# Optimization experiments

Hardware: AMD Instinct MI355X
Metric: run time of the kernel (lower is better)

Reference implementation:

```python
import jax, jax.numpy as jnp
import numpy as np

B, N, D = 512, 128, 128
VALID = 64                      # valid atoms per molecule (structured mask)
N_NODES = B * VALID             # 32768
DEG = 16
N_EDGES = N_NODES * DEG         # 524288
L = 3                           # predictor_layer_num
NUM_TASKS = 12
ATOM_VOCAB, EDGE_VOCAB = 119, 8


def _ln(x, g, b, eps=1e-5):
    mu = jnp.mean(x, -1, keepdims=True)
    v = jnp.mean((x - mu) ** 2, -1, keepdims=True)
    return (x - mu) * jax.lax.rsqrt(v + eps) * g + b


def _gelu(x):
    return jax.nn.gelu(x, approximate=False)  # torch F.gelu default (erf)


def setup_inputs():
    key = jax.random.key(0)
    ks = jax.random.split(key, 40)
    s = 0.02
    d = {}
    d['logits'] = jax.random.normal(ks[0], (B, N, D), jnp.float32)
    d['atom_mask'] = jnp.broadcast_to(jnp.arange(N) < VALID, (B, N))
    d['atom_feature'] = jax.random.randint(ks[1], (N_NODES,), 0, ATOM_VOCAB)
    d['edge_index'] = jax.random.randint(ks[2], (2, N_EDGES), 0, N_NODES)
    d['edge_attr'] = jax.random.randint(ks[3], (N_EDGES,), 0, EDGE_VOCAB)
    d['batch_idx'] = jnp.arange(N_NODES) // VALID
    # GNN encoder params
    d['atom_emb'] = s * jax.random.normal(ks[4], (ATOM_VOCAB, D))
    d['edge_emb'] = s * jax.random.normal(ks[5], (EDGE_VOCAB, D))
    d['gnn_W1'] = s * jax.random.normal(ks[6], (L, D, 2 * D))
    d['gnn_b1'] = jnp.zeros((L, 2 * D))
    d['gnn_W2'] = s * jax.random.normal(ks[7], (L, 2 * D, D))
    d['gnn_b2'] = jnp.zeros((L, D))
    d['gnn_ln_g'] = jnp.ones((L, D))
    d['gnn_ln_b'] = jnp.zeros((L, D))
    # attention pooling gate_nn: Linear(d,2d)->LN->ReLU->Linear(2d,1)
    d['gate_W1'] = s * jax.random.normal(ks[8], (D, 2 * D))
    d['gate_b1'] = jnp.zeros((2 * D,))
    d['gate_ln_g'] = jnp.ones((2 * D,))
    d['gate_ln_b'] = jnp.zeros((2 * D,))
    d['gate_W2'] = s * jax.random.normal(ks[9], (2 * D, 1))
    d['gate_b2'] = jnp.zeros((1,))
    # 2 residual blocks
    d['res_fc1_W'] = s * jax.random.normal(ks[10], (2, D, D))
    d['res_fc1_b'] = jnp.zeros((2, D))
    d['res_ln1_g'] = jnp.ones((2, D))
    d['res_ln1_b'] = jnp.zeros((2, D))
    d['res_fc2_W'] = s * jax.random.normal(ks[11], (2, D, D))
    d['res_fc2_b'] = jnp.zeros((2, D))
    d['res_ln2_g'] = jnp.ones((2, D))
    d['res_ln2_b'] = jnp.zeros((2, D))
    # prediction head
    d['pred_W1'] = s * jax.random.normal(ks[12], (D, D))
    d['pred_b1'] = jnp.zeros((D,))
    d['pred_W2'] = s * jax.random.normal(ks[13], (D, NUM_TASKS))
    d['pred_b2'] = jnp.zeros((NUM_TASKS,))
    return d


def reference(logits, atom_mask, atom_feature, edge_index, edge_attr, batch_idx,
              atom_emb, edge_emb, gnn_W1, gnn_b1, gnn_W2, gnn_b2, gnn_ln_g, gnn_ln_b,
              gate_W1, gate_b1, gate_ln_g, gate_ln_b, gate_W2, gate_b2,
              res_fc1_W, res_fc1_b, res_ln1_g, res_ln1_b,
              res_fc2_W, res_fc2_b, res_ln2_g, res_ln2_b,
              pred_W1, pred_b1, pred_W2, pred_b2):
    # boolean-mask gather: flat_atom_feat[flat_mask] with static masked count
    flat_mask = atom_mask.reshape(-1)
    idx = jnp.nonzero(flat_mask, size=N_NODES)[0]
    x = logits.reshape(-1, D)[idx]                       # [N_NODES, D]
    x = x + atom_emb[atom_feature]                       # incorporate atom features
    src, dst = edge_index[0], edge_index[1]
    e_emb = edge_emb[edge_attr]                          # [E, D]
    # residual GIN-style message passing, JK='last', eval (no dropout)
    for l in range(L):
        msg = jax.nn.relu(x[src] + e_emb)                # [E, D] irregular gather
        agg = jax.ops.segment_sum(msg, dst, num_segments=N_NODES)
        h = jax.nn.relu(agg @ gnn_W1[l] + gnn_b1[l]) @ gnn_W2[l] + gnn_b2[l]
        x = x + _ln(h, gnn_ln_g[l], gnn_ln_b[l])
    # attentional aggregation: segment softmax over nodes per graph
    gate = jax.nn.relu(_ln(x @ gate_W1 + gate_b1, gate_ln_g, gate_ln_b)) @ gate_W2 + gate_b2  # [n,1]
    gm = jax.ops.segment_max(gate, batch_idx, num_segments=B)
    e = jnp.exp(gate - gm[batch_idx])
    den = jax.ops.segment_sum(e, batch_idx, num_segments=B)
    w = e / den[batch_idx]
    g = jax.ops.segment_sum(w * x, batch_idx, num_segments=B)  # [B, D]
    # 2 residual MLP blocks (eval: dropout = identity)
    for r in range(2):
        h = _gelu(_ln(g @ res_fc1_W[r] + res_fc1_b[r], res_ln1_g[r], res_ln1_b[r]))
        h = _ln(h @ res_fc2_W[r] + res_fc2_b[r], res_ln2_g[r], res_ln2_b[r])
        g = g + h
    # prediction head
    return _gelu(g @ pred_W1 + pred_b1) @ pred_W2 + pred_b2  # [B, NUM_TASKS]
```

## Files before the change

### kernel.cpp

```cpp
#include <hip/hip_runtime.h>
#include <hip/hip_bf16.h>

#define N_NODES 32768
#define N_EDGES 524288
#define B_GRAPHS 512

typedef __attribute__((ext_vector_type(8))) short sh8;
typedef __attribute__((ext_vector_type(4))) float f32x4;

__device__ __forceinline__ unsigned short f2b(float f) {
    unsigned int u = __float_as_uint(f);
    return (unsigned short)((u + 0x7FFFu + ((u >> 16) & 1u)) >> 16);
}
__device__ __forceinline__ float blo(unsigned int u) { return __uint_as_float(u << 16); }
__device__ __forceinline__ float bhi(unsigned int u) { return __uint_as_float(u & 0xFFFF0000u); }
__device__ __forceinline__ float gelu_exact(float z) {
    return 0.5f * z * (1.0f + erff(z * 0.70710678118654752440f));
}

__global__ __launch_bounds__(256) void k_prep(const float* __restrict__ W1,
                                              const float* __restrict__ W2,
                                              const float* __restrict__ gW1,
                                              unsigned short* __restrict__ W1T,
                                              unsigned short* __restrict__ W2T,
                                              unsigned short* __restrict__ gW1T,
                                              int* __restrict__ deg) {
    int tid = blockIdx.x * 256 + threadIdx.x;
    if (tid < N_NODES) deg[tid] = 0;
    int m = tid >> 15, i = tid & 32767;
    if (m < 3) {
        int r = i >> 8, c = i & 255;
        W1T[m * 32768 + c * 128 + r] = f2b(W1[m * 32768 + i]);
    } else if (m < 6) {
        int mm = m - 3;
        int r = i >> 7, c = i & 127;
        W2T[mm * 32768 + c * 256 + r] = f2b(W2[mm * 32768 + i]);
    } else {
        int r = i >> 8, c = i & 255;
        gW1T[c * 128 + r] = f2b(gW1[i]);
    }
}

__global__ void k_deg(const int* __restrict__ dst, int* __restrict__ deg) {
    int e = blockIdx.x * blockDim.x + threadIdx.x;
    if (e < N_EDGES) atomicAdd(&deg[dst[e]], 1);
}

__global__ __launch_bounds__(1024) void k_scan(const int* __restrict__ deg,
                                               int* __restrict__ offs,
                                               int* __restrict__ cursor) {
    int tid = threadIdx.x;
    int lane = tid & 63, wid = tid >> 6;
    int base = tid * 32;
    int pref[32];
    int run = 0;
    #pragma unroll
    for (int i = 0; i < 32; i++) { pref[i] = run; run += deg[base + i]; }
    int s = run;
    for (int m = 1; m < 64; m <<= 1) { int t = __shfl_up(s, m); if (lane >= m) s += t; }
    __shared__ int wsum[16];
    if (lane == 63) wsum[wid] = s;
    __syncthreads();
    if (tid < 16) {
        int v = wsum[tid];
        for (int m = 1; m < 16; m <<= 1) { int t = __shfl_up(v, m, 16); if (tid >= m) v += t; }
        wsum[tid] = v;
    }
    __syncthreads();
    int wbase = wid ? wsum[wid - 1] : 0;
    int ebase = wbase + (s - run);
    #pragma unroll
    for (int i = 0; i < 32; i++) {
        int o = ebase + pref[i];
        offs[base + i] = o;
        cursor[base + i] = o;
    }
    if (tid == 1023) offs[N_NODES] = ebase + run;
}

__global__ void k_scatter(const int* __restrict__ src, const int* __restrict__ dst,
                          const int* __restrict__ attr, int* __restrict__ cursor,
                          int* __restrict__ csr) {
    int e = blockIdx.x * blockDim.x + threadIdx.x;
    if (e < N_EDGES) {
        int p = atomicAdd(&cursor[dst[e]], 1);
        csr[p] = src[e] | (attr[e] << 16);
    }
}

__global__ void k_build_x(const float* __restrict__ logits, const int* __restrict__ feat,
                          const float* __restrict__ aemb, float* __restrict__ x,
                          unsigned short* __restrict__ xb) {
    int idx = blockIdx.x * blockDim.x + threadIdx.x;
    int n = idx >> 5, c = idx & 31;
    int srow = ((n >> 6) << 7) + (n & 63);
    float4 lv = ((const float4*)logits)[srow * 32 + c];
    float4 av = ((const float4*)aemb)[feat[n] * 32 + c];
    float4 o;
    o.x = lv.x + av.x; o.y = lv.y + av.y; o.z = lv.z + av.z; o.w = lv.w + av.w;
    ((float4*)x)[idx] = o;
    ushort4 ob;
    ob.x = f2b(o.x); ob.y = f2b(o.y); ob.z = f2b(o.z); ob.w = f2b(o.w);
    ((ushort4*)xb)[idx] = ob;
}

__global__ __launch_bounds__(256) void k_agg(const unsigned short* __restrict__ xb,
                                             const int* __restrict__ offs,
                                             const int* __restrict__ csr,
                                             const float* __restrict__ eemb,
                                             unsigned short* __restrict__ aggb) {
    __shared__ float semb[8 * 128];
    int tid = threadIdx.x;
    for (int i = tid; i < 1024; i += 256) semb[i] = eemb[i];
    __syncthreads();
    int node = blockIdx.x * 4 + (tid >> 6);
    int lane = tid & 63;
    int li = lane & 31, h = lane >> 5;
    int o0 = offs[node], o1 = offs[node + 1];
    float a0 = 0.f, a1 = 0.f, a2 = 0.f, a3 = 0.f;
    int e = o0 + h;
    for (; e + 14 < o1; e += 16) {
        int p[8]; uint2 u[8]; float4 ev[8];
        #pragma unroll
        for (int j = 0; j < 8; j++) p[j] = csr[e + 2 * j];
        #pragma unroll
        for (int j = 0; j < 8; j++)
            u[j] = *(const uint2*)(xb + (size_t)(p[j] & 0xFFFF) * 128 + li * 4);
        #pragma unroll
        for (int j = 0; j < 8; j++)
            ev[j] = *(const float4*)&semb[(p[j] >> 16) * 128 + li * 4];
        #pragma unroll
        for (int j = 0; j < 8; j++) {
            a0 += fmaxf(blo(u[j].x) + ev[j].x, 0.f);
            a1 += fmaxf(bhi(u[j].x) + ev[j].y, 0.f);
            a2 += fmaxf(blo(u[j].y) + ev[j].z, 0.f);
            a3 += fmaxf(bhi(u[j].y) + ev[j].w, 0.f);
        }
    }
    for (; e + 6 < o1; e += 8) {
        int p[4]; uint2 u[4]; float4 ev[4];
        #pragma unroll
        for (int j = 0; j < 4; j++) p[j] = csr[e + 2 * j];
        #pragma unroll
        for (int j = 0; j < 4; j++)
            u[j] = *(const uint2*)(xb + (size_t)(p[j] & 0xFFFF) * 128 + li * 4);
        #pragma unroll
        for (int j = 0; j < 4; j++)
            ev[j] = *(const float4*)&semb[(p[j] >> 16) * 128 + li * 4];
        #pragma unroll
        for (int j = 0; j < 4; j++) {
            a0 += fmaxf(blo(u[j].x) + ev[j].x, 0.f);
            a1 += fmaxf(bhi(u[j].x) + ev[j].y, 0.f);
            a2 += fmaxf(blo(u[j].y) + ev[j].z, 0.f);
            a3 += fmaxf(bhi(u[j].y) + ev[j].w, 0.f);
        }
    }
    for (; e < o1; e += 2) {
        int pk = csr[e];
        uint2 u = *(const uint2*)(xb + (size_t)(pk & 0xFFFF) * 128 + li * 4);
        float4 ev = *(const float4*)&semb[(pk >> 16) * 128 + li * 4];
        a0 += fmaxf(blo(u.x) + ev.x, 0.f); a1 += fmaxf(bhi(u.x) + ev.y, 0.f);
        a2 += fmaxf(blo(u.y) + ev.z, 0.f); a3 += fmaxf(bhi(u.y) + ev.w, 0.f);
    }
    a0 += __shfl_xor(a0, 32); a1 += __shfl_xor(a1, 32);
    a2 += __shfl_xor(a2, 32); a3 += __shfl_xor(a3, 32);
    if (h == 0) {
        uint2 wv;
        wv.x = (unsigned int)f2b(a0) | ((unsigned int)f2b(a1) << 16);
        wv.y = (unsigned int)f2b(a2) | ((unsigned int)f2b(a3) << 16);
        *(uint2*)(aggb + (size_t)node * 128 + li * 4) = wv;
    }
}

__global__ __launch_bounds__(512) void k_layer(const unsigned short* __restrict__ A,
                                               const unsigned short* __restrict__ W1T,
                                               const float* __restrict__ b1,
                                               const unsigned short* __restrict__ W2T,
                                               const float* __restrict__ b2,
                                               const float* __restrict__ lng,
                                               const float* __restrict__ lnb,
                                               float* __restrict__ x,
                                               unsigned short* __restrict__ xb) {
    __shared__ __align__(16) unsigned short WS[33792];
    __shared__ __align__(16) unsigned short T[128][264];
    int tid = threadIdx.x;
    int row0 = blockIdx.x * 128;
    int l = tid & 63, w = tid >> 6;
    int fr = l & 15, hi = l >> 4, fk = hi * 8;
    sh8 afr[4];
    #pragma unroll
    for (int kc = 0; kc < 4; kc++)
        afr[kc] = *(const sh8*)(A + (size_t)(row0 + w * 16 + fr) * 128 + kc * 32 + fk);
    #pragma unroll
    for (int s = tid; s < 4096; s += 512) {
        int n = s >> 4, k8 = s & 15;
        *(uint4*)&WS[n * 132 + k8 * 8] = *(const uint4*)(W1T + (size_t)n * 128 + k8 * 8);
    }
    __syncthreads();
    #pragma unroll
    for (int ch = 0; ch < 2; ch++) {
        f32x4 acc[8];
        #pragma unroll
        for (int c = 0; c < 8; c++) acc[c] = (f32x4){0.f, 0.f, 0.f, 0.f};
        #pragma unroll
        for (int kc = 0; kc < 4; kc++) {
            #pragma unroll
            for (int c = 0; c < 8; c++) {
                sh8 b = *(const sh8*)&WS[(ch * 128 + c * 16 + fr) * 132 + kc * 32 + fk];
                acc[c] = __builtin_amdgcn_mfma_f32_16x16x32_bf16(afr[kc], b, acc[c], 0, 0, 0);
            }
        }
        int rb = w * 16 + hi * 4;
        #pragma unroll
        for (int c = 0; c < 8; c++) {
            int col = ch * 128 + c * 16 + fr;
            float bv = b1[col];
            #pragma unroll
            for (int q = 0; q < 4; q++)
                T[rb + q][col] = f2b(fmaxf(acc[c][q] + bv, 0.f));
        }
    }
    __syncthreads();
    #pragma unroll
    for (int s = tid; s < 4096; s += 512) {
        int n = s >> 5, k8 = s & 31;
        *(uint4*)&WS[n * 264 + k8 * 8] = *(const uint4*)(W2T + (size_t)n * 256 + k8 * 8);
    }
    __syncthreads();
    f32x4 acc[8];
    #pragma unroll
    for (int c = 0; c < 8; c++) acc[c] = (f32x4){0.f, 0.f, 0.f, 0.f};
    #pragma unroll 2
    for (int kc = 0; kc < 8; kc++) {
        sh8 a = *(const sh8*)&T[w * 16 + fr][kc * 32 + fk];
        #pragma unroll
        for (int c = 0; c < 8; c++) {
            sh8 b = *(const sh8*)&WS[(c * 16 + fr) * 264 + kc * 32 + fk];
            acc[c] = __builtin_amdgcn_mfma_f32_16x16x32_bf16(a, b, acc[c], 0, 0, 0);
        }
    }
    float s0 = 0.f, s1 = 0.f, s2 = 0.f, s3 = 0.f;
    float q0 = 0.f, q1 = 0.f, q2 = 0.f, q3 = 0.f;
    #pragma unroll
    for (int c = 0; c < 8; c++) {
        float bv = b2[c * 16 + fr];
        #pragma unroll
        for (int q = 0; q < 4; q++) acc[c][q] += bv;
        s0 += acc[c][0]; q0 += acc[c][0] * acc[c][0];
        s1 += acc[c][1]; q1 += acc[c][1] * acc[c][1];
        s2 += acc[c][2]; q2 += acc[c][2] * acc[c][2];
        s3 += acc[c][3]; q3 += acc[c][3] * acc[c][3];
    }
    #pragma unroll
    for (int m = 1; m < 16; m <<= 1) {
        s0 += __shfl_xor(s0, m); q0 += __shfl_xor(q0, m);
        s1 += __shfl_xor(s1, m); q1 += __shfl_xor(q1, m);
        s2 += __shfl_xor(s2, m); q2 += __shfl_xor(q2, m);
        s3 += __shfl_xor(s3, m); q3 += __shfl_xor(q3, m);
    }
    float mu[4], rs_[4];
    mu[0] = s0 * (1.f / 128.f); rs_[0] = rsqrtf(q0 * (1.f / 128.f) - mu[0] * mu[0] + 1e-5f);
    mu[1] = s1 * (1.f / 128.f); rs_[1] = rsqrtf(q1 * (1.f / 128.f) - mu[1] * mu[1] + 1e-5f);
    mu[2] = s2 * (1.f / 128.f); rs_[2] = rsqrtf(q2 * (1.f / 128.f) - mu[2] * mu[2] + 1e-5f);
    mu[3] = s3 * (1.f / 128.f); rs_[3] = rsqrtf(q3 * (1.f / 128.f) - mu[3] * mu[3] + 1e-5f);
    int rbase = row0 + w * 16 + hi * 4;
    #pragma unroll
    for (int c = 0; c < 8; c++) {
        int col = c * 16 + fr;
        float g = lng[col], bb = lnb[col];
        #pragma unroll
        for (int q = 0; q < 4; q++) {
            size_t idx = (size_t)(rbase + q) * 128 + col;
            float nx = x[idx] + (acc[c][q] - mu[q]) * rs_[q] * g + bb;
            x[idx] = nx;
            xb[idx] = f2b(nx);
        }
    }
}

__global__ __launch_bounds__(512) void k_gatef(const unsigned short* __restrict__ xbin,
                                               const unsigned short* __restrict__ gW1T,
                                               const float* __restrict__ b1,
                                               const float* __restrict__ lng,
                                               const float* __restrict__ lnb,
                                               const float* __restrict__ w2,
                                               const float* __restrict__ b2,
                                               float* __restrict__ gate) {
    __shared__ __align__(16) unsigned short WS[33792];
    __shared__ __align__(16) unsigned short T[128][264];
    int tid = threadIdx.x;
    int row0 = blockIdx.x * 128;
    int l = tid & 63, w = tid >> 6;
    int fr = l & 15, hi = l >> 4, fk = hi * 8;
    sh8 afr[4];
    #pragma unroll
    for (int kc = 0; kc < 4; kc++)
        afr[kc] = *(const sh8*)(xbin + (size_t)(row0 + w * 16 + fr) * 128 + kc * 32 + fk);
    #pragma unroll
    for (int s = tid; s < 4096; s += 512) {
        int n = s >> 4, k8 = s & 15;
        *(uint4*)&WS[n * 132 + k8 * 8] = *(const uint4*)(gW1T + (size_t)n * 128 + k8 * 8);
    }
    __syncthreads();
    #pragma unroll
    for (int ch = 0; ch < 2; ch++) {
        f32x4 acc[8];
        #pragma unroll
        for (int c = 0; c < 8; c++) acc[c] = (f32x4){0.f, 0.f, 0.f, 0.f};
        #pragma unroll
        for (int kc = 0; kc < 4; kc++) {
            #pragma unroll
            for (int c = 0; c < 8; c++) {
                sh8 b = *(const sh8*)&WS[(ch * 128 + c * 16 + fr) * 132 + kc * 32 + fk];
                acc[c] = __builtin_amdgcn_mfma_f32_16x16x32_bf16(afr[kc], b, acc[c], 0, 0, 0);
            }
        }
        int rb = w * 16 + hi * 4;
        #pragma unroll
        for (int c = 0; c < 8; c++) {
            int col = ch * 128 + c * 16 + fr;
            float bv = b1[col];
            #pragma unroll
            for (int q = 0; q < 4; q++)
                T[rb + q][col] = f2b(acc[c][q] + bv);
        }
    }
    __syncthreads();
    int row = tid >> 2, qd = tid & 3;
    float s = 0.f, sq = 0.f;
    #pragma unroll 4
    for (int j = 0; j < 16; j++) {
        uint2 u = *(const uint2*)&T[row][qd * 64 + j * 4];
        float v0 = blo(u.x), v1 = bhi(u.x), v2 = blo(u.y), v3 = bhi(u.y);
        s += v0 + v1 + v2 + v3;
        sq += v0 * v0 + v1 * v1 + v2 * v2 + v3 * v3;
    }
    s += __shfl_xor(s, 1); s += __shfl_xor(s, 2);
    sq += __shfl_xor(sq, 1); sq += __shfl_xor(sq, 2);
    float mu = s * (1.f / 256.f);
    float rcp = rsqrtf(sq * (1.f / 256.f) - mu * mu + 1e-5f);
    float acc = 0.f;
    #pragma unroll 4
    for (int j = 0; j < 16; j++) {
        int col = qd * 64 + j * 4;
        uint2 u = *(const uint2*)&T[row][col];
        float4 g4 = *(const float4*)&lng[col];
        float4 e4 = *(const float4*)&lnb[col];
        float4 w4 = *(const float4*)&w2[col];
        acc += fmaxf((blo(u.x) - mu) * rcp * g4.x + e4.x, 0.f) * w4.x;
        acc += fmaxf((bhi(u.x) - mu) * rcp * g4.y + e4.y, 0.f) * w4.y;
        acc += fmaxf((blo(u.y) - mu) * rcp * g4.z + e4.z, 0.f) * w4.z;
        acc += fmaxf((bhi(u.y) - mu) * rcp * g4.w + e4.w, 0.f) * w4.w;
    }
    acc += __shfl_xor(acc, 1); acc += __shfl_xor(acc, 2);
    if (qd == 0) gate[row0 + row] = acc + b2[0];
}

__global__ __launch_bounds__(256) void k_pool(const float* __restrict__ x,
                                              const float* __restrict__ gate,
                                              float* __restrict__ g) {
    __shared__ float sw[64];
    __shared__ float sacc[128];
    int b = blockIdx.x, tid = threadIdx.x;
    if (tid < 64) {
        float gv = gate[b * 64 + tid];
        float m = gv;
        #pragma unroll
        for (int mk = 1; mk < 64; mk <<= 1) m = fmaxf(m, __shfl_xor(m, mk));
        float e = expf(gv - m);
        float s = e;
        #pragma unroll
        for (int mk = 1; mk < 64; mk <<= 1) s += __shfl_xor(s, mk);
        sw[tid] = e / s;
    }
    __syncthreads();
    int d = tid & 127, h = tid >> 7;
    float acc = 0.f;
    for (int i = h * 32; i < h * 32 + 32; i++)
        acc += sw[i] * x[(size_t)(b * 64 + i) * 128 + d];
    if (h == 0) sacc[d] = acc;
    __syncthreads();
    if (h == 1) g[b * 128 + d] = sacc[d] + acc;
}

__global__ __launch_bounds__(128) void k_tail(const float* __restrict__ g_in,
        const float* __restrict__ fc1W, const float* __restrict__ fc1b,
        const float* __restrict__ ln1g, const float* __restrict__ ln1b,
        const float* __restrict__ fc2W, const float* __restrict__ fc2b,
        const float* __restrict__ ln2g, const float* __restrict__ ln2b,
        const float* __restrict__ pW1, const float* __restrict__ pb1,
        const float* __restrict__ pW2, const float* __restrict__ pb2,
        float* __restrict__ out) {
    __shared__ float sg[128], sh[128];
    __shared__ float ps[2], pq[2];
    int b = blockIdx.x, tid = threadIdx.x;
    int w = tid >> 6;
    sg[tid] = g_in[b * 128 + tid];
    __syncthreads();
    for (int r = 0; r < 2; r++) {
        const float* W1 = fc1W + r * 16384;
        float acc = fc1b[r * 128 + tid];
        for (int k = 0; k < 128; k++) acc += sg[k] * W1[k * 128 + tid];
        float s = acc, q = acc * acc;
        #pragma unroll
        for (int m = 1; m < 64; m <<= 1) { s += __shfl_xor(s, m); q += __shfl_xor(q, m); }
        __syncthreads();
        if ((tid & 63) == 0) { ps[w] = s; pq[w] = q; }
        __syncthreads();
        float S = ps[0] + ps[1], Q = pq[0] + pq[1];
        float mu = S * (1.f / 128.f);
        float var = Q * (1.f / 128.f) - mu * mu;
        float z = (acc - mu) * rsqrtf(var + 1e-5f) * ln1g[r * 128 + tid] + ln1b[r * 128 + tid];
        z = gelu_exact(z);
        __syncthreads();
        sh[tid] = z;
        __syncthreads();
        const float* W2 = fc2W + r * 16384;
        float acc2 = fc2b[r * 128 + tid];
        for (int k = 0; k < 128; k++) acc2 += sh[k] * W2[k * 128 + tid];
        s = acc2; q = acc2 * acc2;
        #pragma unroll
        for (int m = 1; m < 64; m <<= 1) { s += __shfl_xor(s, m); q += __shfl_xor(q, m); }
        __syncthreads();
        if ((tid & 63) == 0) { ps[w] = s; pq[w] = q; }
        __syncthreads();
        S = ps[0] + ps[1]; Q = pq[0] + pq[1];
        mu = S * (1.f / 128.f);
        var = Q * (1.f / 128.f) - mu * mu;
        float z2 = (acc2 - mu) * rsqrtf(var + 1e-5f) * ln2g[r * 128 + tid] + ln2b[r * 128 + tid];
        __syncthreads();
        sg[tid] = sg[tid] + z2;
        __syncthreads();
    }
    float acc = pb1[tid];
    for (int k = 0; k < 128; k++) acc += sg[k] * pW1[k * 128 + tid];
    __syncthreads();
    sh[tid] = gelu_exact(acc);
    __syncthreads();
    if (tid < 12) {
        float o = pb2[tid];
        for (int k = 0; k < 128; k++) o += sh[k] * pW2[k * 12 + tid];
        out[b * 12 + tid] = o;
    }
}

extern "C" void kernel_launch(void* const* d_in, const int* in_sizes, int n_in,
                              void* d_out, int out_size, void* d_ws, size_t ws_size,
                              hipStream_t stream) {
    const float* logits    = (const float*)d_in[0];
    const int*   atom_feat = (const int*)d_in[2];
    const int*   edge_src  = (const int*)d_in[3];
    const int*   edge_dst  = edge_src + N_EDGES;
    const int*   edge_attr = (const int*)d_in[4];
    const float* atom_emb  = (const float*)d_in[6];
    const float* edge_emb  = (const float*)d_in[7];
    const float* gnn_W1    = (const float*)d_in[8];
    const float* gnn_b1    = (const float*)d_in[9];
    const float* gnn_W2    = (const float*)d_in[10];
    const float* gnn_b2    = (const float*)d_in[11];
    const float* gnn_ln_g  = (const float*)d_in[12];
    const float* gnn_ln_b  = (const float*)d_in[13];
    const float* gate_W1   = (const float*)d_in[14];
    const float* gate_b1   = (const float*)d_in[15];
    const float* gate_ln_g = (const float*)d_in[16];
    const float* gate_ln_b = (const float*)d_in[17];
    const float* gate_W2   = (const float*)d_in[18];
    const float* gate_b2   = (const float*)d_in[19];
    const float* res_fc1_W = (const float*)d_in[20];
    const float* res_fc1_b = (const float*)d_in[21];
    const float* res_ln1_g = (const float*)d_in[22];
    const float* res_ln1_b = (const float*)d_in[23];
    const float* res_fc2_W = (const float*)d_in[24];
    const float* res_fc2_b = (const float*)d_in[25];
    const float* res_ln2_g = (const float*)d_in[26];
    const float* res_ln2_b = (const float*)d_in[27];
    const float* pred_W1   = (const float*)d_in[28];
    const float* pred_b1   = (const float*)d_in[29];
    const float* pred_W2   = (const float*)d_in[30];
    const float* pred_b2   = (const float*)d_in[31];
    float* out = (float*)d_out;

    char* w = (char*)d_ws;
    float*          x    = (float*)w;          w += (size_t)N_NODES * 128 * 4;
    unsigned short* xb   = (unsigned short*)w; w += (size_t)N_NODES * 128 * 2;
    unsigned short* aggb = (unsigned short*)w; w += (size_t)N_NODES * 128 * 2;
    unsigned short* W1T  = (unsigned short*)w; w += 3 * 32768 * 2;
    unsigned short* W2T  = (unsigned short*)w; w += 3 * 32768 * 2;
    unsigned short* gW1T = (unsigned short*)w; w += 32768 * 2;
    int*   deg    = (int*)w;   w += N_NODES * 4;
    int*   offs   = (int*)w;   w += (N_NODES + 64) * 4;
    int*   cursor = (int*)w;   w += N_NODES * 4;
    int*   csr    = (int*)w;   w += N_EDGES * 4;
    float* gate   = (float*)w; w += N_NODES * 4;
    float* gpool  = (float*)w; w += B_GRAPHS * 128 * 4;

    k_prep<<<7 * 32768 / 256, 256, 0, stream>>>(gnn_W1, gnn_W2, gate_W1, W1T, W2T, gW1T, deg);
    k_deg<<<N_EDGES / 256, 256, 0, stream>>>(edge_dst, deg);
    k_scan<<<1, 1024, 0, stream>>>(deg, offs, cursor);
    k_scatter<<<N_EDGES / 256, 256, 0, stream>>>(edge_src, edge_dst, edge_attr, cursor, csr);

    k_build_x<<<N_NODES * 32 / 256, 256, 0, stream>>>(logits, atom_feat, atom_emb, x, xb);

    for (int l = 0; l < 3; l++) {
        k_agg<<<N_NODES / 4, 256, 0, stream>>>(xb, offs, csr, edge_emb, aggb);
        k_layer<<<N_NODES / 128, 512, 0, stream>>>(
            aggb, W1T + l * 32768, gnn_b1 + l * 256,
            W2T + l * 32768, gnn_b2 + l * 128,
            gnn_ln_g + l * 128, gnn_ln_b + l * 128, x, xb);
    }

    k_gatef<<<N_NODES / 128, 512, 0, stream>>>(
        xb, gW1T, gate_b1, gate_ln_g, gate_ln_b, gate_W2, gate_b2, gate);

    k_pool<<<B_GRAPHS, 256, 0, stream>>>(x, gate, gpool);

    k_tail<<<B_GRAPHS, 128, 0, stream>>>(gpool,
        res_fc1_W, res_fc1_b, res_ln1_g, res_ln1_b,
        res_fc2_W, res_fc2_b, res_ln2_g, res_ln2_b,
        pred_W1, pred_b1, pred_W2, pred_b2, out);
}
```

Baseline: 281.3 us.

## Fuse gate/pool/tail kernels, merge build_x into prep, split aggregation by feature half

Merges the input-embedding build into the weight-prep kernel, and fuses the gate MLP, segment softmax pooling and the residual/prediction tail into one kernel that handles two graphs per 128-row block. It also splits edge aggregation into two launches, each covering 64 features, with CSR entries loaded once per wave and broadcast by shuffle. The aim is fewer launches, no gate/pool round trips through global memory, and a smaller per-pass gather footprint for better cache hit rates. The cost is a second pass over the CSR indices and more serial, under-occupied tail work inside the fused kernel.

```diff
diff --git a/kernel.cpp b/kernel.cpp
--- a/kernel.cpp
+++ b/kernel.cpp
@@ -18,26 +18,49 @@
     return 0.5f * z * (1.0f + erff(z * 0.70710678118654752440f));
 }
 
+#define PREP_BLOCKS 896
+#define BX_BLOCKS 4096
+
 __global__ __launch_bounds__(256) void k_prep(const float* __restrict__ W1,
                                               const float* __restrict__ W2,
                                               const float* __restrict__ gW1,
+                                              const float* __restrict__ logits,
+                                              const int* __restrict__ feat,
+                                              const float* __restrict__ aemb,
                                               unsigned short* __restrict__ W1T,
                                               unsigned short* __restrict__ W2T,
                                               unsigned short* __restrict__ gW1T,
-                                              int* __restrict__ deg) {
-    int tid = blockIdx.x * 256 + threadIdx.x;
-    if (tid < N_NODES) deg[tid] = 0;
-    int m = tid >> 15, i = tid & 32767;
-    if (m < 3) {
-        int r = i >> 8, c = i & 255;
-        W1T[m * 32768 + c * 128 + r] = f2b(W1[m * 32768 + i]);
-    } else if (m < 6) {
-        int mm = m - 3;
-        int r = i >> 7, c = i & 127;
-        W2T[mm * 32768 + c * 256 + r] = f2b(W2[mm * 32768 + i]);
+                                              int* __restrict__ deg,
+                                              float* __restrict__ x,
+                                              unsigned short* __restrict__ xb) {
+    int bb = blockIdx.x;
+    if (bb < PREP_BLOCKS) {
+        int tid = bb * 256 + threadIdx.x;
+        if (tid < N_NODES) deg[tid] = 0;
+        int m = tid >> 15, i = tid & 32767;
+        if (m < 3) {
+            int r = i >> 8, c = i & 255;
+            W1T[m * 32768 + c * 128 + r] = f2b(W1[m * 32768 + i]);
+        } else if (m < 6) {
+            int mm = m - 3;
+            int r = i >> 7, c = i & 127;
+            W2T[mm * 32768 + c * 256 + r] = f2b(W2[mm * 32768 + i]);
+        } else {
+            int r = i >> 8, c = i & 255;
+            gW1T[c * 128 + r] = f2b(gW1[i]);
+        }
     } else {
-        int r = i >> 8, c = i & 255;
-        gW1T[c * 128 + r] = f2b(gW1[i]);
+        int idx = (bb - PREP_BLOCKS) * 256 + threadIdx.x;
+        int n = idx >> 5, c = idx & 31;
+        int srow = ((n >> 6) << 7) + (n & 63);
+        float4 lv = ((const float4*)logits)[srow * 32 + c];
+        float4 av = ((const float4*)aemb)[feat[n] * 32 + c];
+        float4 o;
+        o.x = lv.x + av.x; o.y = lv.y + av.y; o.z = lv.z + av.z; o.w = lv.w + av.w;
+        ((float4*)x)[idx] = o;
+        ushort4 ob;
+        ob.x = f2b(o.x); ob.y = f2b(o.y); ob.z = f2b(o.z); ob.w = f2b(o.w);
+        ((ushort4*)xb)[idx] = ob;
     }
 }
 
@@ -88,87 +111,66 @@
     }
 }
 
-__global__ void k_build_x(const float* __restrict__ logits, const int* __restrict__ feat,
-                          const float* __restrict__ aemb, float* __restrict__ x,
-                          unsigned short* __restrict__ xb) {
-    int idx = blockIdx.x * blockDim.x + threadIdx.x;
-    int n = idx >> 5, c = idx & 31;
-    int srow = ((n >> 6) << 7) + (n & 63);
-    float4 lv = ((const float4*)logits)[srow * 32 + c];
-    float4 av = ((const float4*)aemb)[feat[n] * 32 + c];
-    float4 o;
-    o.x = lv.x + av.x; o.y = lv.y + av.y; o.z = lv.z + av.z; o.w = lv.w + av.w;
-    ((float4*)x)[idx] = o;
-    ushort4 ob;
-    ob.x = f2b(o.x); ob.y = f2b(o.y); ob.z = f2b(o.z); ob.w = f2b(o.w);
-    ((ushort4*)xb)[idx] = ob;
-}
-
 __global__ __launch_bounds__(256) void k_agg(const unsigned short* __restrict__ xb,
                                              const int* __restrict__ offs,
                                              const int* __restrict__ csr,
                                              const float* __restrict__ eemb,
-                                             unsigned short* __restrict__ aggb) {
-    __shared__ float semb[8 * 128];
+                                             unsigned short* __restrict__ aggb,
+                                             int half) {
+    __shared__ float semb[8 * 64];
     int tid = threadIdx.x;
-    for (int i = tid; i < 1024; i += 256) semb[i] = eemb[i];
+    int fbase = half * 64;
+    for (int i = tid; i < 512; i += 256)
+        semb[i] = eemb[(i >> 6) * 128 + fbase + (i & 63)];
     __syncthreads();
     int node = blockIdx.x * 4 + (tid >> 6);
     int lane = tid & 63;
     int li = lane & 31, h = lane >> 5;
     int o0 = offs[node], o1 = offs[node + 1];
-    float a0 = 0.f, a1 = 0.f, a2 = 0.f, a3 = 0.f;
-    int e = o0 + h;
-    for (; e + 14 < o1; e += 16) {
-        int p[8]; uint2 u[8]; float4 ev[8];
-        #pragma unroll
-        for (int j = 0; j < 8; j++) p[j] = csr[e + 2 * j];
-        #pragma unroll
-        for (int j = 0; j < 8; j++)
-            u[j] = *(const uint2*)(xb + (size_t)(p[j] & 0xFFFF) * 128 + li * 4);
-        #pragma unroll
-        for (int j = 0; j < 8; j++)
-            ev[j] = *(const float4*)&semb[(p[j] >> 16) * 128 + li * 4];
-        #pragma unroll
-        for (int j = 0; j < 8; j++) {
-            a0 += fmaxf(blo(u[j].x) + ev[j].x, 0.f);
-            a1 += fmaxf(bhi(u[j].x) + ev[j].y, 0.f);
-            a2 += fmaxf(blo(u[j].y) + ev[j].z, 0.f);
-            a3 += fmaxf(bhi(u[j].y) + ev[j].w, 0.f);
-        }
-    }
-    for (; e + 6 < o1; e += 8) {
-        int p[4]; uint2 u[4]; float4 ev[4];
-        #pragma unroll
-        for (int j = 0; j < 4; j++) p[j] = csr[e + 2 * j];
-        #pragma unroll
-        for (int j = 0; j < 4; j++)
-            u[j] = *(const uint2*)(xb + (size_t)(p[j] & 0xFFFF) * 128 + li * 4);
-        #pragma unroll
-        for (int j = 0; j < 4; j++)
-            ev[j] = *(const float4*)&semb[(p[j] >> 16) * 128 + li * 4];
-        #pragma unroll
-        for (int j = 0; j < 4; j++) {
-            a0 += fmaxf(blo(u[j].x) + ev[j].x, 0.f);
-            a1 += fmaxf(bhi(u[j].x) + ev[j].y, 0.f);
-            a2 += fmaxf(blo(u[j].y) + ev[j].z, 0.f);
-            a3 += fmaxf(bhi(u[j].y) + ev[j].w, 0.f);
-        }
-    }
-    for (; e < o1; e += 2) {
-        int pk = csr[e];
-        uint2 u = *(const uint2*)(xb + (size_t)(pk & 0xFFFF) * 128 + li * 4);
-        float4 ev = *(const float4*)&semb[(pk >> 16) * 128 + li * 4];
-        a0 += fmaxf(blo(u.x) + ev.x, 0.f); a1 += fmaxf(bhi(u.x) + ev.y, 0.f);
-        a2 += fmaxf(blo(u.y) + ev.z, 0.f); a3 += fmaxf(bhi(u.y) + ev.w, 0.f);
-    }
-    a0 += __shfl_xor(a0, 32); a1 += __shfl_xor(a1, 32);
-    a2 += __shfl_xor(a2, 32); a3 += __shfl_xor(a3, 32);
+    int deg = o1 - o0;
+    int degc = deg < 64 ? deg : 64;
+    int ed = (lane < degc) ? csr[o0 + lane] : 0;
+    float a0 = 0.f, a1 = 0.f;
+    int nh0 = (degc + 1) >> 1;
+    int nhl = h ? (degc >> 1) : nh0;
+    int j = 0;
+    for (; j + 8 <= nh0; j += 8) {
+        int pk[8]; unsigned int u[8];
+        #pragma unroll
+        for (int t = 0; t < 8; t++) pk[t] = __shfl(ed, h + 2 * (j + t));
+        #pragma unroll
+        for (int t = 0; t < 8; t++)
+            u[t] = *(const unsigned int*)(xb + (size_t)(pk[t] & 0xFFFF) * 128 + fbase + li * 2);
+        #pragma unroll
+        for (int t = 0; t < 8; t++) {
+            if (j + t < nhl) {
+                float2 ev = *(const float2*)&semb[(pk[t] >> 16) * 64 + li * 2];
+                a0 += fmaxf(blo(u[t]) + ev.x, 0.f);
+                a1 += fmaxf(bhi(u[t]) + ev.y, 0.f);
+            }
+        }
+    }
+    for (; j < nh0; j++) {
+        int pk = __shfl(ed, h + 2 * j);
+        unsigned int u = *(const unsigned int*)(xb + (size_t)(pk & 0xFFFF) * 128 + fbase + li * 2);
+        if (j < nhl) {
+            float2 ev = *(const float2*)&semb[(pk >> 16) * 64 + li * 2];
+            a0 += fmaxf(blo(u) + ev.x, 0.f);
+            a1 += fmaxf(bhi(u) + ev.y, 0.f);
+        }
+    }
+    for (int i = 64 + h; i < deg; i += 2) {
+        int pk = csr[o0 + i];
+        unsigned int u = *(const unsigned int*)(xb + (size_t)(pk & 0xFFFF) * 128 + fbase + li * 2);
+        float2 ev = *(const float2*)&semb[(pk >> 16) * 64 + li * 2];
+        a0 += fmaxf(blo(u) + ev.x, 0.f);
+        a1 += fmaxf(bhi(u) + ev.y, 0.f);
+    }
+    a0 += __shfl_xor(a0, 32);
+    a1 += __shfl_xor(a1, 32);
     if (h == 0) {
-        uint2 wv;
-        wv.x = (unsigned int)f2b(a0) | ((unsigned int)f2b(a1) << 16);
-        wv.y = (unsigned int)f2b(a2) | ((unsigned int)f2b(a3) << 16);
-        *(uint2*)(aggb + (size_t)node * 128 + li * 4) = wv;
+        unsigned int wv = (unsigned int)f2b(a0) | ((unsigned int)f2b(a1) << 16);
+        *(unsigned int*)(aggb + (size_t)node * 128 + fbase + li * 2) = wv;
     }
 }
 
@@ -278,112 +280,12 @@
     }
 }
 
-__global__ __launch_bounds__(512) void k_gatef(const unsigned short* __restrict__ xbin,
-                                               const unsigned short* __restrict__ gW1T,
-                                               const float* __restrict__ b1,
-                                               const float* __restrict__ lng,
-                                               const float* __restrict__ lnb,
-                                               const float* __restrict__ w2,
-                                               const float* __restrict__ b2,
-                                               float* __restrict__ gate) {
-    __shared__ __align__(16) unsigned short WS[33792];
-    __shared__ __align__(16) unsigned short T[128][264];
-    int tid = threadIdx.x;
-    int row0 = blockIdx.x * 128;
-    int l = tid & 63, w = tid >> 6;
-    int fr = l & 15, hi = l >> 4, fk = hi * 8;
-    sh8 afr[4];
-    #pragma unroll
-    for (int kc = 0; kc < 4; kc++)
-        afr[kc] = *(const sh8*)(xbin + (size_t)(row0 + w * 16 + fr) * 128 + kc * 32 + fk);
-    #pragma unroll
-    for (int s = tid; s < 4096; s += 512) {
-        int n = s >> 4, k8 = s & 15;
-        *(uint4*)&WS[n * 132 + k8 * 8] = *(const uint4*)(gW1T + (size_t)n * 128 + k8 * 8);
-    }
-    __syncthreads();
-    #pragma unroll
-    for (int ch = 0; ch < 2; ch++) {
-        f32x4 acc[8];
-        #pragma unroll
-        for (int c = 0; c < 8; c++) acc[c] = (f32x4){0.f, 0.f, 0.f, 0.f};
-        #pragma unroll
-        for (int kc = 0; kc < 4; kc++) {
-            #pragma unroll
-            for (int c = 0; c < 8; c++) {
-                sh8 b = *(const sh8*)&WS[(ch * 128 + c * 16 + fr) * 132 + kc * 32 + fk];
-                acc[c] = __builtin_amdgcn_mfma_f32_16x16x32_bf16(afr[kc], b, acc[c], 0, 0, 0);
-            }
-        }
-        int rb = w * 16 + hi * 4;
-        #pragma unroll
-        for (int c = 0; c < 8; c++) {
-            int col = ch * 128 + c * 16 + fr;
-            float bv = b1[col];
-            #pragma unroll
-            for (int q = 0; q < 4; q++)
-                T[rb + q][col] = f2b(acc[c][q] + bv);
-        }
-    }
-    __syncthreads();
-    int row = tid >> 2, qd = tid & 3;
-    float s = 0.f, sq = 0.f;
-    #pragma unroll 4
-    for (int j = 0; j < 16; j++) {
-        uint2 u = *(const uint2*)&T[row][qd * 64 + j * 4];
-        float v0 = blo(u.x), v1 = bhi(u.x), v2 = blo(u.y), v3 = bhi(u.y);
-        s += v0 + v1 + v2 + v3;
-        sq += v0 * v0 + v1 * v1 + v2 * v2 + v3 * v3;
-    }
-    s += __shfl_xor(s, 1); s += __shfl_xor(s, 2);
-    sq += __shfl_xor(sq, 1); sq += __shfl_xor(sq, 2);
-    float mu = s * (1.f / 256.f);
-    float rcp = rsqrtf(sq * (1.f / 256.f) - mu * mu + 1e-5f);
-    float acc = 0.f;
-    #pragma unroll 4
-    for (int j = 0; j < 16; j++) {
-        int col = qd * 64 + j * 4;
-        uint2 u = *(const uint2*)&T[row][col];
-        float4 g4 = *(const float4*)&lng[col];
-        float4 e4 = *(const float4*)&lnb[col];
-        float4 w4 = *(const float4*)&w2[col];
-        acc += fmaxf((blo(u.x) - mu) * rcp * g4.x + e4.x, 0.f) * w4.x;
-        acc += fmaxf((bhi(u.x) - mu) * rcp * g4.y + e4.y, 0.f) * w4.y;
-        acc += fmaxf((blo(u.y) - mu) * rcp * g4.z + e4.z, 0.f) * w4.z;
-        acc += fmaxf((bhi(u.y) - mu) * rcp * g4.w + e4.w, 0.f) * w4.w;
-    }
-    acc += __shfl_xor(acc, 1); acc += __shfl_xor(acc, 2);
-    if (qd == 0) gate[row0 + row] = acc + b2[0];
-}
-
-__global__ __launch_bounds__(256) void k_pool(const float* __restrict__ x,
-                                              const float* __restrict__ gate,
-                                              float* __restrict__ g) {
-    __shared__ float sw[64];
-    __shared__ float sacc[128];
-    int b = blockIdx.x, tid = threadIdx.x;
-    if (tid < 64) {
-        float gv = gate[b * 64 + tid];
-        float m = gv;
-        #pragma unroll
-        for (int mk = 1; mk < 64; mk <<= 1) m = fmaxf(m, __shfl_xor(m, mk));
-        float e = expf(gv - m);
-        float s = e;
-        #pragma unroll
-        for (int mk = 1; mk < 64; mk <<= 1) s += __shfl_xor(s, mk);
-        sw[tid] = e / s;
-    }
-    __syncthreads();
-    int d = tid & 127, h = tid >> 7;
-    float acc = 0.f;
-    for (int i = h * 32; i < h * 32 + 32; i++)
-        acc += sw[i] * x[(size_t)(b * 64 + i) * 128 + d];
-    if (h == 0) sacc[d] = acc;
-    __syncthreads();
-    if (h == 1) g[b * 128 + d] = sacc[d] + acc;
-}
-
-__global__ __launch_bounds__(128) void k_tail(const float* __restrict__ g_in,
+__global__ __launch_bounds__(512) void k_gpt(const unsigned short* __restrict__ xbin,
+        const float* __restrict__ xf,
+        const unsigned short* __restrict__ gW1T,
+        const float* __restrict__ b1,
+        const float* __restrict__ lng, const float* __restrict__ lnb,
+        const float* __restrict__ w2, const float* __restrict__ b2,
         const float* __restrict__ fc1W, const float* __restrict__ fc1b,
         const float* __restrict__ ln1g, const float* __restrict__ ln1b,
         const float* __restrict__ fc2W, const float* __restrict__ fc2b,
@@ -391,56 +293,155 @@
         const float* __restrict__ pW1, const float* __restrict__ pb1,
         const float* __restrict__ pW2, const float* __restrict__ pb2,
         float* __restrict__ out) {
-    __shared__ float sg[128], sh[128];
-    __shared__ float ps[2], pq[2];
-    int b = blockIdx.x, tid = threadIdx.x;
-    int w = tid >> 6;
-    sg[tid] = g_in[b * 128 + tid];
-    __syncthreads();
+    __shared__ __align__(16) unsigned short WS[33792];
+    __shared__ __align__(16) unsigned short T[128][264];
+    __shared__ float gates[128];
+    __shared__ float pooled[2][128];
+    __shared__ float shh[2][128];
+    __shared__ float ps[2][2], pq[2][2];
+    int tid = threadIdx.x;
+    int row0 = blockIdx.x * 128;
+    int l = tid & 63, w = tid >> 6;
+    int fr = l & 15, hi = l >> 4, fk = hi * 8;
+    sh8 afr[4];
+    #pragma unroll
+    for (int kc = 0; kc < 4; kc++)
+        afr[kc] = *(const sh8*)(xbin + (size_t)(row0 + w * 16 + fr) * 128 + kc * 32 + fk);
+    #pragma unroll
+    for (int s = tid; s < 4096; s += 512) {
+        int n = s >> 4, k8 = s & 15;
+        *(uint4*)&WS[n * 132 + k8 * 8] = *(const uint4*)(gW1T + (size_t)n * 128 + k8 * 8);
+    }
+    __syncthreads();
+    #pragma unroll
+    for (int ch = 0; ch < 2; ch++) {
+        f32x4 acc[8];
+        #pragma unroll
+        for (int c = 0; c < 8; c++) acc[c] = (f32x4){0.f, 0.f, 0.f, 0.f};
+        #pragma unroll
+        for (int kc = 0; kc < 4; kc++) {
+            #pragma unroll
+            for (int c = 0; c < 8; c++) {
+                sh8 b = *(const sh8*)&WS[(ch * 128 + c * 16 + fr) * 132 + kc * 32 + fk];
+                acc[c] = __builtin_amdgcn_mfma_f32_16x16x32_bf16(afr[kc], b, acc[c], 0, 0, 0);
+            }
+        }
+        int rb = w * 16 + hi * 4;
+        #pragma unroll
+        for (int c = 0; c < 8; c++) {
+            int col = ch * 128 + c * 16 + fr;
+            float bv = b1[col];
+            #pragma unroll
+            for (int q = 0; q < 4; q++)
+                T[rb + q][col] = f2b(acc[c][q] + bv);
+        }
+    }
+    __syncthreads();
+    {
+        int row = tid >> 2, qd = tid & 3;
+        float s = 0.f, sq = 0.f;
+        #pragma unroll 4
+        for (int j = 0; j < 16; j++) {
+            uint2 u = *(const uint2*)&T[row][qd * 64 + j * 4];
+            float v0 = blo(u.x), v1 = bhi(u.x), v2 = blo(u.y), v3 = bhi(u.y);
+            s += v0 + v1 + v2 + v3;
+            sq += v0 * v0 + v1 * v1 + v2 * v2 + v3 * v3;
+        }
+        s += __shfl_xor(s, 1); s += __shfl_xor(s, 2);
+        sq += __shfl_xor(sq, 1); sq += __shfl_xor(sq, 2);
+        float mu = s * (1.f / 256.f);
+        float rcp = rsqrtf(sq * (1.f / 256.f) - mu * mu + 1e-5f);
+        float acc = 0.f;
+        #pragma unroll 4
+        for (int j = 0; j < 16; j++) {
+            int col = qd * 64 + j * 4;
+            uint2 u = *(const uint2*)&T[row][col];
+            float4 g4 = *(const float4*)&lng[col];
+            float4 e4 = *(const float4*)&lnb[col];
+            float4 w4 = *(const float4*)&w2[col];
+            acc += fmaxf((blo(u.x) - mu) * rcp * g4.x + e4.x, 0.f) * w4.x;
+            acc += fmaxf((bhi(u.x) - mu) * rcp * g4.y + e4.y, 0.f) * w4.y;
+            acc += fmaxf((blo(u.y) - mu) * rcp * g4.z + e4.z, 0.f) * w4.z;
+            acc += fmaxf((bhi(u.y) - mu) * rcp * g4.w + e4.w, 0.f) * w4.w;
+        }
+        acc += __shfl_xor(acc, 1); acc += __shfl_xor(acc, 2);
+        if (qd == 0) gates[row] = acc + b2[0];
+    }
+    __syncthreads();
+    int g = tid >> 8, t2 = tid & 255;
+    if (t2 < 64) {
+        float gv = gates[g * 64 + t2];
+        float m = gv;
+        #pragma unroll
+        for (int mk = 1; mk < 64; mk <<= 1) m = fmaxf(m, __shfl_xor(m, mk));
+        float e = expf(gv - m);
+        float s = e;
+        #pragma unroll
+        for (int mk = 1; mk < 64; mk <<= 1) s += __shfl_xor(s, mk);
+        gates[g * 64 + t2] = e / s;
+    }
+    __syncthreads();
+    int d = t2 & 127, hh = t2 >> 7;
+    float pacc = 0.f;
+    for (int i = hh * 32; i < hh * 32 + 32; i++)
+        pacc += gates[g * 64 + i] * xf[(size_t)(row0 + g * 64 + i) * 128 + d];
+    if (hh == 0) pooled[g][d] = pacc;
+    __syncthreads();
+    if (hh == 1) pooled[g][d] += pacc;
+    __syncthreads();
+    int wv = t2 >> 6;
     for (int r = 0; r < 2; r++) {
-        const float* W1 = fc1W + r * 16384;
-        float acc = fc1b[r * 128 + tid];
-        for (int k = 0; k < 128; k++) acc += sg[k] * W1[k * 128 + tid];
-        float s = acc, q = acc * acc;
-        #pragma unroll
-        for (int m = 1; m < 64; m <<= 1) { s += __shfl_xor(s, m); q += __shfl_xor(q, m); }
+        float acc = 0.f, s = 0.f, q = 0.f;
+        if (t2 < 128) {
+            const float* W1 = fc1W + r * 16384;
+            acc = fc1b[r * 128 + t2];
+            for (int k = 0; k < 128; k++) acc += pooled[g][k] * W1[k * 128 + t2];
+            s = acc; q = acc * acc;
+            #pragma unroll
+            for (int m = 1; m < 64; m <<= 1) { s += __shfl_xor(s, m); q += __shfl_xor(q, m); }
+            if ((t2 & 63) == 0) { ps[g][wv] = s; pq[g][wv] = q; }
+        }
         __syncthreads();
-        if ((tid & 63) == 0) { ps[w] = s; pq[w] = q; }
+        if (t2 < 128) {
+            float S = ps[g][0] + ps[g][1], Q = pq[g][0] + pq[g][1];
+            float mu = S * (1.f / 128.f);
+            float var = Q * (1.f / 128.f) - mu * mu;
+            float z = (acc - mu) * rsqrtf(var + 1e-5f) * ln1g[r * 128 + t2] + ln1b[r * 128 + t2];
+            shh[g][t2] = gelu_exact(z);
+        }
         __syncthreads();
-        float S = ps[0] + ps[1], Q = pq[0] + pq[1];
-        float mu = S * (1.f / 128.f);
-        float var = Q * (1.f / 128.f) - mu * mu;
-        float z = (acc - mu) * rsqrtf(var + 1e-5f) * ln1g[r * 128 + tid] + ln1b[r * 128 + tid];
-        z = gelu_exact(z);
+        float acc2 = 0.f;
+        if (t2 < 128) {
+            const float* W2 = fc2W + r * 16384;
+            acc2 = fc2b[r * 128 + t2];
+            for (int k = 0; k < 128; k++) acc2 += shh[g][k] * W2[k * 128 + t2];
+            s = acc2; q = acc2 * acc2;
+            #pragma unroll
+            for (int m = 1; m < 64; m <<= 1) { s += __shfl_xor(s, m); q += __shfl_xor(q, m); }
+            if ((t2 & 63) == 0) { ps[g][wv] = s; pq[g][wv] = q; }
+        }
         __syncthreads();
-        sh[tid] = z;
+        if (t2 < 128) {
+            float S = ps[g][0] + ps[g][1], Q = pq[g][0] + pq[g][1];
+            float mu = S * (1.f / 128.f);
+            float var = Q * (1.f / 128.f) - mu * mu;
+            float z2 = (acc2 - mu) * rsqrtf(var + 1e-5f) * ln2g[r * 128 + t2] + ln2b[r * 128 + t2];
+            pooled[g][t2] = pooled[g][t2] + z2;
+        }
         __syncthreads();
-        const float* W2 = fc2W + r * 16384;
-        float acc2 = fc2b[r * 128 + tid];
-        for (int k = 0; k < 128; k++) acc2 += sh[k] * W2[k * 128 + tid];
-        s = acc2; q = acc2 * acc2;
-        #pragma unroll
-        for (int m = 1; m < 64; m <<= 1) { s += __shfl_xor(s, m); q += __shfl_xor(q, m); }
-        __syncthreads();
-        if ((tid & 63) == 0) { ps[w] = s; pq[w] = q; }
-        __syncthreads();
-        S = ps[0] + ps[1]; Q = pq[0] + pq[1];
-        mu = S * (1.f / 128.f);
-        var = Q * (1.f / 128.f) - mu * mu;
-        float z2 = (acc2 - mu) * rsqrtf(var + 1e-5f) * ln2g[r * 128 + tid] + ln2b[r * 128 + tid];
-        __syncthreads();
-        sg[tid] = sg[tid] + z2;
-        __syncthreads();
-    }
-    float acc = pb1[tid];
-    for (int k = 0; k < 128; k++) acc += sg[k] * pW1[k * 128 + tid];
-    __syncthreads();
-    sh[tid] = gelu_exact(acc);
-    __syncthreads();
-    if (tid < 12) {
-        float o = pb2[tid];
-        for (int k = 0; k < 128; k++) o += sh[k] * pW2[k * 12 + tid];
-        out[b * 12 + tid] = o;
+    }
+    float hacc = 0.f;
+    if (t2 < 128) {
+        hacc = pb1[t2];
+        for (int k = 0; k < 128; k++) hacc += pooled[g][k] * pW1[k * 128 + t2];
+    }
+    __syncthreads();
+    if (t2 < 128) shh[g][t2] = gelu_exact(hacc);
+    __syncthreads();
+    if (t2 < 12) {
+        float o = pb2[t2];
+        for (int k = 0; k < 128; k++) o += shh[g][k] * pW2[k * 12 + t2];
+        out[(size_t)(blockIdx.x * 2 + g) * 12 + t2] = o;
     }
 }
 
@@ -491,30 +492,25 @@
     int*   offs   = (int*)w;   w += (N_NODES + 64) * 4;
     int*   cursor = (int*)w;   w += N_NODES * 4;
     int*   csr    = (int*)w;   w += N_EDGES * 4;
-    float* gate   = (float*)w; w += N_NODES * 4;
-    float* gpool  = (float*)w; w += B_GRAPHS * 128 * 4;
-
-    k_prep<<<7 * 32768 / 256, 256, 0, stream>>>(gnn_W1, gnn_W2, gate_W1, W1T, W2T, gW1T, deg);
+
+    k_prep<<<PREP_BLOCKS + BX_BLOCKS, 256, 0, stream>>>(
+        gnn_W1, gnn_W2, gate_W1, logits, atom_feat, atom_emb,
+        W1T, W2T, gW1T, deg, x, xb);
     k_deg<<<N_EDGES / 256, 256, 0, stream>>>(edge_dst, deg);
     k_scan<<<1, 1024, 0, stream>>>(deg, offs, cursor);
     k_scatter<<<N_EDGES / 256, 256, 0, stream>>>(edge_src, edge_dst, edge_attr, cursor, csr);
 
-    k_build_x<<<N_NODES * 32 / 256, 256, 0, stream>>>(logits, atom_feat, atom_emb, x, xb);
-
     for (int l = 0; l < 3; l++) {
-        k_agg<<<N_NODES / 4, 256, 0, stream>>>(xb, offs, csr, edge_emb, aggb);
+        k_agg<<<N_NODES / 4, 256, 0, stream>>>(xb, offs, csr, edge_emb, aggb, 0);
+        k_agg<<<N_NODES / 4, 256, 0, stream>>>(xb, offs, csr, edge_emb, aggb, 1);
         k_layer<<<N_NODES / 128, 512, 0, stream>>>(
             aggb, W1T + l * 32768, gnn_b1 + l * 256,
             W2T + l * 32768, gnn_b2 + l * 128,
             gnn_ln_g + l * 128, gnn_ln_b + l * 128, x, xb);
     }
 
-    k_gatef<<<N_NODES / 128, 512, 0, stream>>>(
-        xb, gW1T, gate_b1, gate_ln_g, gate_ln_b, gate_W2, gate_b2, gate);
-
-    k_pool<<<B_GRAPHS, 256, 0, stream>>>(x, gate, gpool);
-
-    k_tail<<<B_GRAPHS, 128, 0, stream>>>(gpool,
+    k_gpt<<<N_NODES / 128, 512, 0, stream>>>(
+        xb, x, gW1T, gate_b1, gate_ln_g, gate_ln_b, gate_W2, gate_b2,
         res_fc1_W, res_fc1_b, res_ln1_g, res_ln1_b,
         res_fc2_W, res_fc2_b, res_ln2_g, res_ln2_b,
         pred_W1, pred_b1, pred_W2, pred_b2, out);
```

New measurement: 303.4 us. 1.08x slower.
